# Performance work log

Measured on AMD Instinct MI355X. Metric: run time of the kernel, lower is better.

Reference implementation:

```python
import jax, jax.numpy as jnp
import numpy as np

B, C, H, W = 32, 64, 32, 32
N = H * W  # 1024 spatial positions


def setup_inputs() -> dict:
    key = jax.random.key(0)
    ks = jax.random.split(key, 7)
    s_c = 1.0 / np.sqrt(C)
    s_n = 1.0 / np.sqrt(N)
    return {
        "x": jax.random.normal(ks[0], (B, C, H, W), dtype=jnp.float32),
        "w_phi": jax.random.normal(ks[1], (C, C), dtype=jnp.float32) * s_c,
        "w_theta": jax.random.normal(ks[2], (C, C), dtype=jnp.float32) * s_c,
        "w_g": jax.random.normal(ks[3], (C, C), dtype=jnp.float32) * s_c,
        "w_mask": jax.random.normal(ks[4], (C, C), dtype=jnp.float32) * s_c,
        "w_mv": jax.random.normal(ks[5], (C, C), dtype=jnp.float32) * s_c,
        "w_mk": jax.random.normal(ks[6], (N, N), dtype=jnp.float32) * s_n,
    }


def reference(x, w_phi, w_theta, w_g, w_mask, w_mv, w_mk):
    b, c, h, w = x.shape
    n = h * w
    xf = x.reshape(b, c, n)  # [b, c, N]
    # 1x1 convs == channel GEMMs (weight layout [out, in])
    phi = jnp.einsum("oc,bcn->bon", w_phi, xf)      # [b, c, N]
    theta = jnp.einsum("oc,bcn->bno", w_theta, xf)  # [b, N, c]
    g = jnp.einsum("oc,bcn->bno", w_g, xf)          # [b, N, c]
    # mv: Linear(c, c) on last dim of g  (y = g @ W^T)
    g = jnp.einsum("bnc,dc->bnd", g, w_mv)
    # theta @ phi -> [b, N, N]
    att = jnp.einsum("bnc,bcm->bnm", theta, phi)
    # mk: Linear(N, N) on last dim
    att = jnp.einsum("bnm,km->bnk", att, w_mk)
    # softmax over dim=1 (rows of the NxN map)
    att = jax.nn.softmax(att, axis=1)
    # att @ g -> [b, N, c]
    out = jnp.einsum("bnm,bmc->bnc", att, g)
    out = out.transpose(0, 2, 1).reshape(b, c, h, w)
    mask = jnp.einsum("oc,bchw->bohw", w_mask, out)
    return mask + x
```

## Files before the change

kernel.cpp:

```cpp
#include <hip/hip_runtime.h>

#define BB 32
#define CC 64
#define NN 1024

typedef __attribute__((ext_vector_type(8))) short bf8;
typedef __attribute__((ext_vector_type(4))) float f4;
typedef __attribute__((ext_vector_type(4))) unsigned short us4;

__device__ __forceinline__ unsigned short f2bf(float f) {
    unsigned u = __float_as_uint(f);
    return (unsigned short)((u + 0x7fffu + ((u >> 16) & 1u)) >> 16);
}
__device__ __forceinline__ float bf2f(unsigned short u) {
    return __uint_as_float(((unsigned)u) << 16);
}

#define MFMA(a, b, c) __builtin_amdgcn_mfma_f32_16x16x32_bf16(a, b, c, 0, 0, 0)

#define GLDS(g, l)                                                              \
    __builtin_amdgcn_global_load_lds(                                           \
        (const __attribute__((address_space(1))) void*)(g),                     \
        (__attribute__((address_space(3))) void*)(l), 16, 0, 0)

__global__ void k0_prep(const float* __restrict__ w_mv, const float* __restrict__ w_g,
                        const float* __restrict__ w_theta, const float* __restrict__ w_phi,
                        const float* __restrict__ w_mask,
                        unsigned short* __restrict__ wcat_bf,
                        unsigned short* __restrict__ wmask_bf) {
    int idx = blockIdx.x * 256 + threadIdx.x;
    int d = idx >> 6, e = idx & 63;
    float acc = 0.f;
    for (int c = 0; c < 64; ++c) acc += w_mv[d * 64 + c] * w_g[c * 64 + e];
    wcat_bf[idx] = f2bf(w_theta[idx]);
    wcat_bf[4096 + idx] = f2bf(w_phi[idx]);
    wcat_bf[8192 + idx] = f2bf(acc);
    wmask_bf[idx] = f2bf(w_mask[idx]);
}

__global__ void k0b_wmk(const float* __restrict__ wmk, unsigned short* __restrict__ wmk_bf) {
    int i = (blockIdx.x * 256 + threadIdx.x) * 4;
    float4 v = *(const float4*)(wmk + i);
    us4 r;
    r.x = f2bf(v.x); r.y = f2bf(v.y); r.z = f2bf(v.z); r.w = f2bf(v.w);
    *(us4*)(wmk_bf + i) = r;
}

__global__ __launch_bounds__(256, 4) void k1_channel(const float* __restrict__ x,
                                                     const unsigned short* __restrict__ wcat,
                                                     unsigned short* __restrict__ theta_nc,
                                                     unsigned short* __restrict__ phi_cm,
                                                     unsigned short* __restrict__ g2_cm) {
    __shared__ unsigned short xT[64][66];
    int b = blockIdx.y;
    int n0 = blockIdx.x * 64;
    int tid = threadIdx.x;
    int w = tid >> 6, lane = tid & 63, l16 = lane & 15, q = lane >> 4;
    size_t bo = (size_t)b * CC * NN;
#pragma unroll
    for (int i = 0; i < 16; ++i) {
        int idx = i * 256 + tid;
        int c = idx >> 6, n2 = idx & 63;
        xT[n2][c] = f2bf(x[bo + (size_t)c * NN + n0 + n2]);
    }
    __syncthreads();
    bf8 bF[4][2];
#pragma unroll
    for (int ct = 0; ct < 4; ++ct) {
        bF[ct][0] = *(const bf8*)&xT[ct * 16 + l16][q * 8];
        bF[ct][1] = *(const bf8*)&xT[ct * 16 + l16][32 + q * 8];
    }
#pragma unroll
    for (int rt = 0; rt < 3; ++rt) {
        int R = w * 48 + rt * 16;
        const unsigned short* wa = wcat + (R + l16) * 64 + q * 8;
        bf8 a0 = *(const bf8*)wa;
        bf8 a1 = *(const bf8*)(wa + 32);
        int which = R >> 6, rb = R & 63;
#pragma unroll
        for (int ct = 0; ct < 4; ++ct) {
            f4 acc = {0.f, 0.f, 0.f, 0.f};
            acc = MFMA(a0, bF[ct][0], acc);
            acc = MFMA(a1, bF[ct][1], acc);
            int n = n0 + ct * 16 + l16;
            if (which == 0) {
                us4 t;
                t.x = f2bf(acc[0]); t.y = f2bf(acc[1]);
                t.z = f2bf(acc[2]); t.w = f2bf(acc[3]);
                *(us4*)&theta_nc[bo + (size_t)n * 64 + rb + q * 4] = t;
            } else {
                unsigned short* dst = (which == 1 ? phi_cm : g2_cm) + bo;
#pragma unroll
                for (int r = 0; r < 4; ++r)
                    dst[(size_t)(rb + q * 4 + r) * NN + n] = f2bf(acc[r]);
            }
        }
    }
}

__global__ __launch_bounds__(512, 4) void k2_phi2(const unsigned short* __restrict__ phi_cm,
                                                  const unsigned short* __restrict__ wmk_bf,
                                                  unsigned short* __restrict__ phi2t) {
    __shared__ unsigned short bT[2][4096];
    __shared__ float red[64][68];
    int b = blockIdx.y;
    int k0 = blockIdx.x * 64;
    int tid = threadIdx.x;
    int w = tid >> 6, lane = tid & 63, l16 = lane & 15, q = lane >> 4;
    int e8 = lane >> 3, c8 = (lane & 7) * 8;
    int ks = w & 3, mh = w >> 2;
    size_t bo = (size_t)b * CC * NN;
    const unsigned short* phib = phi_cm + bo;
    const unsigned short* arow = wmk_bf + (size_t)(k0 + ks * 16 + l16) * NN + q * 8;
    f4 acc[4];
#pragma unroll
    for (int tc = 0; tc < 4; ++tc) acc[tc] = (f4){0.f, 0.f, 0.f, 0.f};

#pragma unroll 1
    for (int mc = 0; mc < 8; ++mc) {
        int m0 = mh * 512 + mc * 64;
        bf8 a0 = *(const bf8*)(arow + m0);
        bf8 a1 = *(const bf8*)(arow + m0 + 32);
        __syncthreads();
        const unsigned short* gg = phib + (size_t)(ks * 16 + e8) * NN + m0 + c8;
        GLDS(gg, &bT[mh][ks * 1024]);
        GLDS(gg + (size_t)8 * NN, &bT[mh][ks * 1024 + 512]);
        __syncthreads();
#pragma unroll
        for (int tc = 0; tc < 4; ++tc) {
            bf8 b0 = *(const bf8*)&bT[mh][(tc * 16 + l16) * 64 + q * 8];
            bf8 b1 = *(const bf8*)&bT[mh][(tc * 16 + l16) * 64 + 32 + q * 8];
            acc[tc] = MFMA(a0, b0, acc[tc]);
            acc[tc] = MFMA(a1, b1, acc[tc]);
        }
    }
    __syncthreads();
    if (mh == 1) {
#pragma unroll
        for (int tc = 0; tc < 4; ++tc)
#pragma unroll
            for (int r = 0; r < 4; ++r) red[ks * 16 + q * 4 + r][tc * 16 + l16] = acc[tc][r];
    }
    __syncthreads();
    if (mh == 0) {
        unsigned short* prow = phi2t + bo;
#pragma unroll
        for (int tc = 0; tc < 4; ++tc)
#pragma unroll
            for (int r = 0; r < 4; ++r) {
                float v = acc[tc][r] + red[ks * 16 + q * 4 + r][tc * 16 + l16];
                prow[(size_t)(k0 + ks * 16 + q * 4 + r) * 64 + tc * 16 + l16] = f2bf(v);
            }
    }
}

__global__ __launch_bounds__(512, 4) void k3_stats(const unsigned short* __restrict__ theta_nc,
                                                   const unsigned short* __restrict__ phi2t,
                                                   const unsigned short* __restrict__ g2_cm,
                                                   unsigned short* __restrict__ g3_cm) {
    __shared__ float sred[8][64];
    __shared__ float svs[64];
    int b = blockIdx.y;
    int k0 = blockIdx.x * 64;
    int tid = threadIdx.x;
    int w = tid >> 6, lane = tid & 63, l16 = lane & 15, q = lane >> 4;
    int wq = w & 3, nh = w >> 2;
    size_t bo = (size_t)b * CC * NN;
    bf8 bF[4][2];
#pragma unroll
    for (int tc = 0; tc < 4; ++tc)
#pragma unroll
        for (int kc = 0; kc < 2; ++kc)
            bF[tc][kc] = *(const bf8*)(phi2t + bo + (size_t)(k0 + tc * 16 + l16) * 64 + kc * 32 + q * 8);
    float s[4] = {0.f, 0.f, 0.f, 0.f};
    const unsigned short* thb = theta_nc + bo + q * 8;
    int nbase = nh * 8;
    int nrow0 = (nbase + 0) * 64 + wq * 16 + l16;
    bf8 a0 = *(const bf8*)(thb + (size_t)nrow0 * 64);
    bf8 a1 = *(const bf8*)(thb + (size_t)nrow0 * 64 + 32);
    for (int nb = 0; nb < 8; ++nb) {
        bf8 p0, p1;
        if (nb < 7) {
            int nr = (nbase + nb + 1) * 64 + wq * 16 + l16;
            p0 = *(const bf8*)(thb + (size_t)nr * 64);
            p1 = *(const bf8*)(thb + (size_t)nr * 64 + 32);
        }
#pragma unroll
        for (int tc = 0; tc < 4; ++tc) {
            f4 acc = {0.f, 0.f, 0.f, 0.f};
            acc = MFMA(a0, bF[tc][0], acc);
            acc = MFMA(a1, bF[tc][1], acc);
            s[tc] += __expf(acc[0]) + __expf(acc[1]) + __expf(acc[2]) + __expf(acc[3]);
        }
        a0 = p0;
        a1 = p1;
    }
#pragma unroll
    for (int tc = 0; tc < 4; ++tc) {
        s[tc] += __shfl_xor(s[tc], 16, 64);
        s[tc] += __shfl_xor(s[tc], 32, 64);
    }
    if (q == 0) {
#pragma unroll
        for (int tc = 0; tc < 4; ++tc) sred[w][tc * 16 + l16] = s[tc];
    }
    __syncthreads();
    if (tid < 64) {
        float S = 0.f;
#pragma unroll
        for (int ww = 0; ww < 8; ++ww) S += sred[ww][tid];
        svs[tid] = 1.f / S;
    }
    __syncthreads();
    int c0 = tid >> 6, kl = tid & 63;
#pragma unroll
    for (int i = 0; i < 8; ++i) {
        int c = c0 * 8 + i;
        size_t ix = bo + (size_t)c * NN + k0 + kl;
        g3_cm[ix] = f2bf(bf2f(g2_cm[ix]) * svs[kl]);
    }
}

__global__ __launch_bounds__(512, 4) void k4_out(const unsigned short* __restrict__ theta_nc,
                                                 const unsigned short* __restrict__ phi2t,
                                                 const unsigned short* __restrict__ g3_cm,
                                                 const unsigned short* __restrict__ wmask_bf,
                                                 const float* __restrict__ x,
                                                 float* __restrict__ out) {
    __shared__ unsigned short stage[16384];
    __shared__ unsigned short P_lds[2][64][72];
    __shared__ unsigned short o_lds[64][72];
    int b = blockIdx.y;
    int n0 = blockIdx.x * 64;
    int tid = threadIdx.x;
    int w = tid >> 6, lane = tid & 63, l16 = lane & 15, q = lane >> 4;
    int e8 = lane >> 3, c8 = (lane & 7) * 8;
    int ws = w & 3, mh = w >> 2;
    int nl = ws * 16 + l16;
    size_t bo = (size_t)b * CC * NN;
    unsigned short* aT = stage + mh * 4096;
    unsigned short* gT = stage + 8192 + mh * 4096;
    bf8 thB[2];
#pragma unroll
    for (int kc = 0; kc < 2; ++kc)
        thB[kc] = *(const bf8*)(theta_nc + bo + (size_t)(n0 + nl) * 64 + kc * 32 + q * 8);
    f4 accO[4];
#pragma unroll
    for (int tr = 0; tr < 4; ++tr) accO[tr] = (f4){0.f, 0.f, 0.f, 0.f};
    const unsigned short* p2b = phi2t + bo;
    const unsigned short* g3b = g3_cm + bo;

#pragma unroll 1
    for (int mc = 0; mc < 8; ++mc) {
        int m0 = mh * 512 + mc * 64;
        __syncthreads();
        {
            int r = ws * 16 + e8;
            const unsigned short* ga = p2b + (size_t)(m0 + r) * 64 + c8;
            GLDS(ga, aT + ws * 1024);
            GLDS(ga + 8 * 64, aT + ws * 1024 + 512);
            const unsigned short* gg = g3b + (size_t)r * NN + m0 + c8;
            GLDS(gg, gT + ws * 1024);
            GLDS(gg + (size_t)8 * NN, gT + ws * 1024 + 512);
        }
        __syncthreads();
#pragma unroll
        for (int tr = 0; tr < 4; ++tr) {
            int row = (tr * 16 + l16) * 64;
            bf8 a0 = *(const bf8*)&aT[row + q * 8];
            bf8 a1 = *(const bf8*)&aT[row + 32 + q * 8];
            f4 at = {0.f, 0.f, 0.f, 0.f};
            at = MFMA(a0, thB[0], at);
            at = MFMA(a1, thB[1], at);
            us4 pk;
            pk.x = f2bf(__expf(at[0]));
            pk.y = f2bf(__expf(at[1]));
            pk.z = f2bf(__expf(at[2]));
            pk.w = f2bf(__expf(at[3]));
            *(us4*)&P_lds[mh][nl][tr * 16 + q * 4] = pk;
        }
        bf8 pF0 = *(const bf8*)&P_lds[mh][nl][q * 8];
        bf8 pF1 = *(const bf8*)&P_lds[mh][nl][32 + q * 8];
#pragma unroll
        for (int tr = 0; tr < 4; ++tr) {
            int row = (tr * 16 + l16) * 64;
            bf8 g0 = *(const bf8*)&gT[row + q * 8];
            bf8 g1 = *(const bf8*)&gT[row + 32 + q * 8];
            accO[tr] = MFMA(g0, pF0, accO[tr]);
            accO[tr] = MFMA(g1, pF1, accO[tr]);
        }
    }
    __syncthreads();
    float (*o_red)[68] = (float(*)[68])(void*)stage;
    if (mh == 1) {
#pragma unroll
        for (int tr = 0; tr < 4; ++tr)
#pragma unroll
            for (int r = 0; r < 4; ++r) o_red[tr * 16 + q * 4 + r][nl] = accO[tr][r];
    }
    __syncthreads();
    if (mh == 0) {
#pragma unroll
        for (int tr = 0; tr < 4; ++tr) {
            us4 ov;
            ov.x = f2bf(accO[tr][0] + o_red[tr * 16 + q * 4 + 0][nl]);
            ov.y = f2bf(accO[tr][1] + o_red[tr * 16 + q * 4 + 1][nl]);
            ov.z = f2bf(accO[tr][2] + o_red[tr * 16 + q * 4 + 2][nl]);
            ov.w = f2bf(accO[tr][3] + o_red[tr * 16 + q * 4 + 3][nl]);
            *(us4*)&o_lds[nl][tr * 16 + q * 4] = ov;
        }
    }
    __syncthreads();
    bf8 oB0 = *(const bf8*)&o_lds[nl][q * 8];
    bf8 oB1 = *(const bf8*)&o_lds[nl][32 + q * 8];
#pragma unroll
    for (int t2 = 0; t2 < 2; ++t2) {
        int tr = mh * 2 + t2;
        const unsigned short* wa = wmask_bf + (tr * 16 + l16) * 64 + q * 8;
        bf8 w0 = *(const bf8*)wa;
        bf8 w1 = *(const bf8*)(wa + 32);
        f4 accF = {0.f, 0.f, 0.f, 0.f};
        accF = MFMA(w0, oB0, accF);
        accF = MFMA(w1, oB1, accF);
#pragma unroll
        for (int r = 0; r < 4; ++r) {
            size_t ix = bo + (size_t)(tr * 16 + q * 4 + r) * NN + n0 + nl;
            out[ix] = accF[r] + x[ix];
        }
    }
}

extern "C" void kernel_launch(void* const* d_in, const int* in_sizes, int n_in,
                              void* d_out, int out_size, void* d_ws, size_t ws_size,
                              hipStream_t stream) {
    const float* x       = (const float*)d_in[0];
    const float* w_phi   = (const float*)d_in[1];
    const float* w_theta = (const float*)d_in[2];
    const float* w_g     = (const float*)d_in[3];
    const float* w_mask  = (const float*)d_in[4];
    const float* w_mv    = (const float*)d_in[5];
    const float* w_mk    = (const float*)d_in[6];
    float* out = (float*)d_out;

    const size_t CN = (size_t)BB * CC * NN;
    char* p = (char*)d_ws;
    unsigned short* theta_nc = (unsigned short*)p; p += CN * 2;
    unsigned short* phi_cm = (unsigned short*)p;   p += CN * 2;
    unsigned short* g2_cm = (unsigned short*)p;    p += CN * 2;
    unsigned short* g3_cm = (unsigned short*)p;    p += CN * 2;
    unsigned short* phi2t = (unsigned short*)p;    p += CN * 2;
    unsigned short* wmk_bf = (unsigned short*)p;   p += (size_t)NN * NN * 2;
    unsigned short* wcat_bf = (unsigned short*)p;  p += 192 * 64 * 2;
    unsigned short* wmask_bf = (unsigned short*)p; p += 4096 * 2;

    k0_prep<<<16, 256, 0, stream>>>(w_mv, w_g, w_theta, w_phi, w_mask, wcat_bf, wmask_bf);
    k0b_wmk<<<1024, 256, 0, stream>>>(w_mk, wmk_bf);
    k1_channel<<<dim3(16, BB), 256, 0, stream>>>(x, wcat_bf, theta_nc, phi_cm, g2_cm);
    k2_phi2<<<dim3(16, BB), 512, 0, stream>>>(phi_cm, wmk_bf, phi2t);
    k3_stats<<<dim3(16, BB), 512, 0, stream>>>(theta_nc, phi2t, g2_cm, g3_cm);
    k4_out<<<dim3(16, BB), 512, 0, stream>>>(theta_nc, phi2t, g3_cm, wmask_bf, x, out);
}
```

Baseline: 139.0 us.

## Fold mask weight into g projection and materialize exp attention matrix

Precomputes w_mask·w_mv·w_g so the final mask GEMM is absorbed into the g path, removing the epilogue MFMA stage in the output kernel. The stats kernel now writes the full exponentiated attention matrix E (B×N×N bf16) to workspace, and the output kernel reads E instead of recomputing theta·phi2 and exp. This trades recomputation for a large extra memory write and read, about 64MB each way, and runs the weight prep as a single block.

```diff
diff --git a/kernel.cpp b/kernel.cpp
--- a/kernel.cpp
+++ b/kernel.cpp
@@ -23,19 +23,33 @@
         (const __attribute__((address_space(1))) void*)(g),                     \
         (__attribute__((address_space(3))) void*)(l), 16, 0, 0)
 
-__global__ void k0_prep(const float* __restrict__ w_mv, const float* __restrict__ w_g,
-                        const float* __restrict__ w_theta, const float* __restrict__ w_phi,
-                        const float* __restrict__ w_mask,
-                        unsigned short* __restrict__ wcat_bf,
-                        unsigned short* __restrict__ wmask_bf) {
-    int idx = blockIdx.x * 256 + threadIdx.x;
-    int d = idx >> 6, e = idx & 63;
-    float acc = 0.f;
-    for (int c = 0; c < 64; ++c) acc += w_mv[d * 64 + c] * w_g[c * 64 + e];
-    wcat_bf[idx] = f2bf(w_theta[idx]);
-    wcat_bf[4096 + idx] = f2bf(w_phi[idx]);
-    wcat_bf[8192 + idx] = f2bf(acc);
-    wmask_bf[idx] = f2bf(w_mask[idx]);
+__global__ __launch_bounds__(1024) void k0_prep(const float* __restrict__ w_mv,
+                                                const float* __restrict__ w_g,
+                                                const float* __restrict__ w_theta,
+                                                const float* __restrict__ w_phi,
+                                                const float* __restrict__ w_mask,
+                                                unsigned short* __restrict__ wcat_bf) {
+    __shared__ float t[4096];
+    int tid = threadIdx.x;
+#pragma unroll
+    for (int i = 0; i < 4; ++i) {
+        int idx = i * 1024 + tid;
+        int d = idx >> 6, e = idx & 63;
+        float acc = 0.f;
+        for (int c = 0; c < 64; ++c) acc += w_mv[d * 64 + c] * w_g[c * 64 + e];
+        t[idx] = acc;
+        wcat_bf[idx] = f2bf(w_theta[idx]);
+        wcat_bf[4096 + idx] = f2bf(w_phi[idx]);
+    }
+    __syncthreads();
+#pragma unroll
+    for (int i = 0; i < 4; ++i) {
+        int idx = i * 1024 + tid;
+        int d = idx >> 6, e = idx & 63;
+        float acc = 0.f;
+        for (int c = 0; c < 64; ++c) acc += w_mask[d * 64 + c] * t[c * 64 + e];
+        wcat_bf[8192 + idx] = f2bf(acc);
+    }
 }
 
 __global__ void k0b_wmk(const float* __restrict__ wmk, unsigned short* __restrict__ wmk_bf) {
@@ -50,7 +64,7 @@
                                                      const unsigned short* __restrict__ wcat,
                                                      unsigned short* __restrict__ theta_nc,
                                                      unsigned short* __restrict__ phi_cm,
-                                                     unsigned short* __restrict__ g2_cm) {
+                                                     unsigned short* __restrict__ g4raw_cm) {
     __shared__ unsigned short xT[64][66];
     int b = blockIdx.y;
     int n0 = blockIdx.x * 64;
@@ -89,7 +103,7 @@
                 t.z = f2bf(acc[2]); t.w = f2bf(acc[3]);
                 *(us4*)&theta_nc[bo + (size_t)n * 64 + rb + q * 4] = t;
             } else {
-                unsigned short* dst = (which == 1 ? phi_cm : g2_cm) + bo;
+                unsigned short* dst = (which == 1 ? phi_cm : g4raw_cm) + bo;
 #pragma unroll
                 for (int r = 0; r < 4; ++r)
                     dst[(size_t)(rb + q * 4 + r) * NN + n] = f2bf(acc[r]);
@@ -156,8 +170,9 @@
 
 __global__ __launch_bounds__(512, 4) void k3_stats(const unsigned short* __restrict__ theta_nc,
                                                    const unsigned short* __restrict__ phi2t,
-                                                   const unsigned short* __restrict__ g2_cm,
-                                                   unsigned short* __restrict__ g3_cm) {
+                                                   const unsigned short* __restrict__ g4raw,
+                                                   unsigned short* __restrict__ E,
+                                                   unsigned short* __restrict__ g4) {
     __shared__ float sred[8][64];
     __shared__ float svs[64];
     int b = blockIdx.y;
@@ -166,43 +181,61 @@
     int w = tid >> 6, lane = tid & 63, l16 = lane & 15, q = lane >> 4;
     int wq = w & 3, nh = w >> 2;
     size_t bo = (size_t)b * CC * NN;
-    bf8 bF[4][2];
+    size_t eo = (size_t)b * NN * NN;
+    bf8 aF[4][2];
 #pragma unroll
     for (int tc = 0; tc < 4; ++tc)
 #pragma unroll
         for (int kc = 0; kc < 2; ++kc)
-            bF[tc][kc] = *(const bf8*)(phi2t + bo + (size_t)(k0 + tc * 16 + l16) * 64 + kc * 32 + q * 8);
-    float s[4] = {0.f, 0.f, 0.f, 0.f};
+            aF[tc][kc] = *(const bf8*)(phi2t + bo + (size_t)(k0 + tc * 16 + l16) * 64 + kc * 32 + q * 8);
+    float sacc[4][4];
+#pragma unroll
+    for (int tc = 0; tc < 4; ++tc)
+#pragma unroll
+        for (int r = 0; r < 4; ++r) sacc[tc][r] = 0.f;
     const unsigned short* thb = theta_nc + bo + q * 8;
     int nbase = nh * 8;
-    int nrow0 = (nbase + 0) * 64 + wq * 16 + l16;
-    bf8 a0 = *(const bf8*)(thb + (size_t)nrow0 * 64);
-    bf8 a1 = *(const bf8*)(thb + (size_t)nrow0 * 64 + 32);
+    int nrow0 = nbase * 64 + wq * 16 + l16;
+    bf8 t0 = *(const bf8*)(thb + (size_t)nrow0 * 64);
+    bf8 t1 = *(const bf8*)(thb + (size_t)nrow0 * 64 + 32);
     for (int nb = 0; nb < 8; ++nb) {
+        int n = (nbase + nb) * 64 + wq * 16 + l16;
         bf8 p0, p1;
         if (nb < 7) {
-            int nr = (nbase + nb + 1) * 64 + wq * 16 + l16;
+            int nr = n + 64;
             p0 = *(const bf8*)(thb + (size_t)nr * 64);
             p1 = *(const bf8*)(thb + (size_t)nr * 64 + 32);
         }
 #pragma unroll
         for (int tc = 0; tc < 4; ++tc) {
             f4 acc = {0.f, 0.f, 0.f, 0.f};
-            acc = MFMA(a0, bF[tc][0], acc);
-            acc = MFMA(a1, bF[tc][1], acc);
-            s[tc] += __expf(acc[0]) + __expf(acc[1]) + __expf(acc[2]) + __expf(acc[3]);
-        }
-        a0 = p0;
-        a1 = p1;
-    }
-#pragma unroll
-    for (int tc = 0; tc < 4; ++tc) {
-        s[tc] += __shfl_xor(s[tc], 16, 64);
-        s[tc] += __shfl_xor(s[tc], 32, 64);
-    }
-    if (q == 0) {
-#pragma unroll
-        for (int tc = 0; tc < 4; ++tc) sred[w][tc * 16 + l16] = s[tc];
+            acc = MFMA(aF[tc][0], t0, acc);
+            acc = MFMA(aF[tc][1], t1, acc);
+            float e0 = __expf(acc[0]), e1 = __expf(acc[1]);
+            float e2 = __expf(acc[2]), e3 = __expf(acc[3]);
+            us4 ev;
+            ev.x = f2bf(e0); ev.y = f2bf(e1); ev.z = f2bf(e2); ev.w = f2bf(e3);
+            *(us4*)&E[eo + (size_t)n * NN + k0 + tc * 16 + q * 4] = ev;
+            sacc[tc][0] += e0; sacc[tc][1] += e1;
+            sacc[tc][2] += e2; sacc[tc][3] += e3;
+        }
+        t0 = p0;
+        t1 = p1;
+    }
+#pragma unroll
+    for (int tc = 0; tc < 4; ++tc)
+#pragma unroll
+        for (int r = 0; r < 4; ++r) {
+            sacc[tc][r] += __shfl_xor(sacc[tc][r], 1, 64);
+            sacc[tc][r] += __shfl_xor(sacc[tc][r], 2, 64);
+            sacc[tc][r] += __shfl_xor(sacc[tc][r], 4, 64);
+            sacc[tc][r] += __shfl_xor(sacc[tc][r], 8, 64);
+        }
+    if (l16 == 0) {
+#pragma unroll
+        for (int tc = 0; tc < 4; ++tc)
+#pragma unroll
+            for (int r = 0; r < 4; ++r) sred[w][tc * 16 + q * 4 + r] = sacc[tc][r];
     }
     __syncthreads();
     if (tid < 64) {
@@ -217,116 +250,75 @@
     for (int i = 0; i < 8; ++i) {
         int c = c0 * 8 + i;
         size_t ix = bo + (size_t)c * NN + k0 + kl;
-        g3_cm[ix] = f2bf(bf2f(g2_cm[ix]) * svs[kl]);
-    }
-}
-
-__global__ __launch_bounds__(512, 4) void k4_out(const unsigned short* __restrict__ theta_nc,
-                                                 const unsigned short* __restrict__ phi2t,
-                                                 const unsigned short* __restrict__ g3_cm,
-                                                 const unsigned short* __restrict__ wmask_bf,
+        g4[ix] = f2bf(bf2f(g4raw[ix]) * svs[kl]);
+    }
+}
+
+__global__ __launch_bounds__(512, 4) void k4_out(const unsigned short* __restrict__ E,
+                                                 const unsigned short* __restrict__ g4,
                                                  const float* __restrict__ x,
                                                  float* __restrict__ out) {
-    __shared__ unsigned short stage[16384];
-    __shared__ unsigned short P_lds[2][64][72];
-    __shared__ unsigned short o_lds[64][72];
+    __shared__ char smem[32768];
+    unsigned short* st = (unsigned short*)smem;
     int b = blockIdx.y;
     int n0 = blockIdx.x * 64;
     int tid = threadIdx.x;
     int w = tid >> 6, lane = tid & 63, l16 = lane & 15, q = lane >> 4;
     int e8 = lane >> 3, c8 = (lane & 7) * 8;
-    int ws = w & 3, mh = w >> 2;
-    int nl = ws * 16 + l16;
+    int os = w & 3, mh = w >> 2;
     size_t bo = (size_t)b * CC * NN;
-    unsigned short* aT = stage + mh * 4096;
-    unsigned short* gT = stage + 8192 + mh * 4096;
-    bf8 thB[2];
-#pragma unroll
-    for (int kc = 0; kc < 2; ++kc)
-        thB[kc] = *(const bf8*)(theta_nc + bo + (size_t)(n0 + nl) * 64 + kc * 32 + q * 8);
-    f4 accO[4];
-#pragma unroll
-    for (int tr = 0; tr < 4; ++tr) accO[tr] = (f4){0.f, 0.f, 0.f, 0.f};
-    const unsigned short* p2b = phi2t + bo;
-    const unsigned short* g3b = g3_cm + bo;
+    size_t eo = (size_t)b * NN * NN;
+    const unsigned short* g4b = g4 + bo;
+    const unsigned short* Eb = E + eo;
+    unsigned short* aT = st + mh * 4096;
+    unsigned short* bT = st + 8192 + mh * 4096;
+    f4 acc[4];
+#pragma unroll
+    for (int ct = 0; ct < 4; ++ct) acc[ct] = (f4){0.f, 0.f, 0.f, 0.f};
 
 #pragma unroll 1
     for (int mc = 0; mc < 8; ++mc) {
         int m0 = mh * 512 + mc * 64;
         __syncthreads();
         {
-            int r = ws * 16 + e8;
-            const unsigned short* ga = p2b + (size_t)(m0 + r) * 64 + c8;
-            GLDS(ga, aT + ws * 1024);
-            GLDS(ga + 8 * 64, aT + ws * 1024 + 512);
-            const unsigned short* gg = g3b + (size_t)r * NN + m0 + c8;
-            GLDS(gg, gT + ws * 1024);
-            GLDS(gg + (size_t)8 * NN, gT + ws * 1024 + 512);
+            int r = os * 16 + e8;
+            const unsigned short* ga = g4b + (size_t)r * NN + m0 + c8;
+            GLDS(ga, aT + os * 1024);
+            GLDS(ga + (size_t)8 * NN, aT + os * 1024 + 512);
+            const unsigned short* ge = Eb + (size_t)(n0 + r) * NN + m0 + c8;
+            GLDS(ge, bT + os * 1024);
+            GLDS(ge + (size_t)8 * NN, bT + os * 1024 + 512);
         }
         __syncthreads();
-#pragma unroll
-        for (int tr = 0; tr < 4; ++tr) {
-            int row = (tr * 16 + l16) * 64;
-            bf8 a0 = *(const bf8*)&aT[row + q * 8];
-            bf8 a1 = *(const bf8*)&aT[row + 32 + q * 8];
-            f4 at = {0.f, 0.f, 0.f, 0.f};
-            at = MFMA(a0, thB[0], at);
-            at = MFMA(a1, thB[1], at);
-            us4 pk;
-            pk.x = f2bf(__expf(at[0]));
-            pk.y = f2bf(__expf(at[1]));
-            pk.z = f2bf(__expf(at[2]));
-            pk.w = f2bf(__expf(at[3]));
-            *(us4*)&P_lds[mh][nl][tr * 16 + q * 4] = pk;
-        }
-        bf8 pF0 = *(const bf8*)&P_lds[mh][nl][q * 8];
-        bf8 pF1 = *(const bf8*)&P_lds[mh][nl][32 + q * 8];
-#pragma unroll
-        for (int tr = 0; tr < 4; ++tr) {
-            int row = (tr * 16 + l16) * 64;
-            bf8 g0 = *(const bf8*)&gT[row + q * 8];
-            bf8 g1 = *(const bf8*)&gT[row + 32 + q * 8];
-            accO[tr] = MFMA(g0, pF0, accO[tr]);
-            accO[tr] = MFMA(g1, pF1, accO[tr]);
-        }
-    }
-    __syncthreads();
-    float (*o_red)[68] = (float(*)[68])(void*)stage;
+        bf8 a0 = *(const bf8*)&aT[(os * 16 + l16) * 64 + q * 8];
+        bf8 a1 = *(const bf8*)&aT[(os * 16 + l16) * 64 + 32 + q * 8];
+#pragma unroll
+        for (int ct = 0; ct < 4; ++ct) {
+            bf8 b0 = *(const bf8*)&bT[(ct * 16 + l16) * 64 + q * 8];
+            bf8 b1 = *(const bf8*)&bT[(ct * 16 + l16) * 64 + 32 + q * 8];
+            acc[ct] = MFMA(a0, b0, acc[ct]);
+            acc[ct] = MFMA(a1, b1, acc[ct]);
+        }
+    }
+    __syncthreads();
+    float (*red)[68] = (float(*)[68])(void*)smem;
     if (mh == 1) {
 #pragma unroll
-        for (int tr = 0; tr < 4; ++tr)
-#pragma unroll
-            for (int r = 0; r < 4; ++r) o_red[tr * 16 + q * 4 + r][nl] = accO[tr][r];
+        for (int ct = 0; ct < 4; ++ct)
+#pragma unroll
+            for (int r = 0; r < 4; ++r) red[os * 16 + q * 4 + r][ct * 16 + l16] = acc[ct][r];
     }
     __syncthreads();
     if (mh == 0) {
 #pragma unroll
-        for (int tr = 0; tr < 4; ++tr) {
-            us4 ov;
-            ov.x = f2bf(accO[tr][0] + o_red[tr * 16 + q * 4 + 0][nl]);
-            ov.y = f2bf(accO[tr][1] + o_red[tr * 16 + q * 4 + 1][nl]);
-            ov.z = f2bf(accO[tr][2] + o_red[tr * 16 + q * 4 + 2][nl]);
-            ov.w = f2bf(accO[tr][3] + o_red[tr * 16 + q * 4 + 3][nl]);
-            *(us4*)&o_lds[nl][tr * 16 + q * 4] = ov;
-        }
-    }
-    __syncthreads();
-    bf8 oB0 = *(const bf8*)&o_lds[nl][q * 8];
-    bf8 oB1 = *(const bf8*)&o_lds[nl][32 + q * 8];
-#pragma unroll
-    for (int t2 = 0; t2 < 2; ++t2) {
-        int tr = mh * 2 + t2;
-        const unsigned short* wa = wmask_bf + (tr * 16 + l16) * 64 + q * 8;
-        bf8 w0 = *(const bf8*)wa;
-        bf8 w1 = *(const bf8*)(wa + 32);
-        f4 accF = {0.f, 0.f, 0.f, 0.f};
-        accF = MFMA(w0, oB0, accF);
-        accF = MFMA(w1, oB1, accF);
-#pragma unroll
-        for (int r = 0; r < 4; ++r) {
-            size_t ix = bo + (size_t)(tr * 16 + q * 4 + r) * NN + n0 + nl;
-            out[ix] = accF[r] + x[ix];
-        }
+        for (int ct = 0; ct < 4; ++ct)
+#pragma unroll
+            for (int r = 0; r < 4; ++r) {
+                int o = os * 16 + q * 4 + r;
+                int n = ct * 16 + l16;
+                size_t ix = bo + (size_t)o * NN + n0 + n;
+                out[ix] = acc[ct][r] + red[o][n] + x[ix];
+            }
     }
 }
 
@@ -346,17 +338,17 @@
     char* p = (char*)d_ws;
     unsigned short* theta_nc = (unsigned short*)p; p += CN * 2;
     unsigned short* phi_cm = (unsigned short*)p;   p += CN * 2;
-    unsigned short* g2_cm = (unsigned short*)p;    p += CN * 2;
-    unsigned short* g3_cm = (unsigned short*)p;    p += CN * 2;
+    unsigned short* g4raw = (unsigned short*)p;    p += CN * 2;
+    unsigned short* g4 = (unsigned short*)p;       p += CN * 2;
     unsigned short* phi2t = (unsigned short*)p;    p += CN * 2;
     unsigned short* wmk_bf = (unsigned short*)p;   p += (size_t)NN * NN * 2;
     unsigned short* wcat_bf = (unsigned short*)p;  p += 192 * 64 * 2;
-    unsigned short* wmask_bf = (unsigned short*)p; p += 4096 * 2;
-
-    k0_prep<<<16, 256, 0, stream>>>(w_mv, w_g, w_theta, w_phi, w_mask, wcat_bf, wmask_bf);
+    unsigned short* E = (unsigned short*)p;        p += (size_t)BB * NN * NN * 2;
+
+    k0_prep<<<1, 1024, 0, stream>>>(w_mv, w_g, w_theta, w_phi, w_mask, wcat_bf);
     k0b_wmk<<<1024, 256, 0, stream>>>(w_mk, wmk_bf);
-    k1_channel<<<dim3(16, BB), 256, 0, stream>>>(x, wcat_bf, theta_nc, phi_cm, g2_cm);
+    k1_channel<<<dim3(16, BB), 256, 0, stream>>>(x, wcat_bf, theta_nc, phi_cm, g4raw);
     k2_phi2<<<dim3(16, BB), 512, 0, stream>>>(phi_cm, wmk_bf, phi2t);
-    k3_stats<<<dim3(16, BB), 512, 0, stream>>>(theta_nc, phi2t, g2_cm, g3_cm);
-    k4_out<<<dim3(16, BB), 512, 0, stream>>>(theta_nc, phi2t, g3_cm, wmask_bf, x, out);
-}
+    k3_stats<<<dim3(16, BB), 512, 0, stream>>>(theta_nc, phi2t, g4raw, E, g4);
+    k4_out<<<dim3(16, BB), 512, 0, stream>>>(E, g4, x, out);
+}
```

Measured after the change: 192.0 us. 1.38x slower.
